# Kernel tuning notes

Measured on AMD Instinct MI355X. Metric: run time of the kernel, lower is better.

## Reference

```python
import jax, jax.numpy as jnp
import numpy as np

EMB = 1024
HEADS = 16


def setup_inputs() -> dict:
    key = jax.random.key(0)
    k1, k2, k3, k4, k5 = jax.random.split(key, 5)
    b, n = 2, 2048
    x = jax.random.normal(k1, (b, n, EMB), dtype=jnp.float32)
    Wqkv = jax.random.normal(k2, (EMB, 3 * EMB), dtype=jnp.float32) * (EMB ** -0.5)
    bqkv = jax.random.normal(k3, (3 * EMB,), dtype=jnp.float32) * 0.02
    Wproj = jax.random.normal(k4, (EMB, EMB), dtype=jnp.float32) * (EMB ** -0.5)
    bproj = jax.random.normal(k5, (EMB,), dtype=jnp.float32) * 0.02
    return {"x": x, "Wqkv": Wqkv, "bqkv": bqkv, "Wproj": Wproj, "bproj": bproj}


def reference(x, Wqkv, bqkv, Wproj, bproj):
    b, n, e = x.shape
    h = HEADS
    d = e // h
    qkv = x @ Wqkv + bqkv                      # [b, n, 3e]
    # rearrange 'b n (h d qkv) -> qkv b h n d' : qkv index is innermost
    qkv = qkv.reshape(b, n, h, d, 3)
    qkv = jnp.transpose(qkv, (4, 0, 2, 1, 3))  # [3, b, h, n, d]
    q, k, v = qkv[0], qkv[1], qkv[2]
    energy = jnp.einsum('bhqd,bhkd->bhqk', q, k)
    scaling = jnp.float32(e) ** 0.5            # NOTE: sqrt(emb_size), not head_dim
    att = jax.nn.softmax(energy / scaling, axis=-1)
    out = jnp.einsum('bhql,bhld->bhqd', att, v)
    out = jnp.transpose(out, (0, 2, 1, 3)).reshape(b, n, e)  # 'b h n d -> b n (h d)'
    return out @ Wproj + bproj
```

## Files before the change

kernel.cpp:

```cpp
#include <hip/hip_runtime.h>
#include <hip/hip_bf16.h>
#include <stdint.h>

typedef __bf16 bf16;
typedef __attribute__((ext_vector_type(8))) __bf16 bf16x8;
typedef __attribute__((ext_vector_type(4))) __bf16 bf16x4;
typedef __attribute__((ext_vector_type(4))) float f32x4;
typedef __attribute__((ext_vector_type(16))) float f32x16;

#define MFMA16(a, b, c) __builtin_amdgcn_mfma_f32_16x16x32_bf16((a), (b), (c), 0, 0, 0)
#define MFMA32(a, b, c) __builtin_amdgcn_mfma_f32_32x32x16_bf16((a), (b), (c), 0, 0, 0)

#define QSCALE 0.045084220027780106f

__device__ __forceinline__ void glds16(const void* g, void* l) {
  __builtin_amdgcn_global_load_lds(
      (const __attribute__((address_space(1))) void*)g,
      (__attribute__((address_space(3))) void*)l, 16, 0, 0);
}

__device__ __forceinline__ bf16x8 ldsfrag(const unsigned char* base, int row, int colb) {
  return *(const bf16x8*)(base + row * 128 + (colb ^ ((row & 7) << 4)));
}

__device__ __forceinline__ uint32_t pkbf16(float a, float b) {
  uint32_t r;
  asm("v_cvt_pk_bf16_f32 %0, %1, %2" : "=v"(r) : "v"(a), "v"(b));
  return r;
}

__device__ __forceinline__ float fexp2(float x) {
#if __has_builtin(__builtin_amdgcn_exp2f)
  return __builtin_amdgcn_exp2f(x);
#else
  float r;
  asm("v_exp_f32 %0, %1" : "=v"(r) : "v"(x));
  return r;
#endif
}

__device__ __forceinline__ f32x16 zero16() {
  f32x16 v;
#pragma unroll
  for (int i = 0; i < 16; ++i) v[i] = 0.f;
  return v;
}

template <int MODE>
__device__ __forceinline__ void prep_w_body(const float* __restrict__ W, bf16* __restrict__ WT,
                                            float (*tile)[256], int c0, int k0) {
  const int C = (MODE == 0) ? 3072 : 1024;
  const int lw = threadIdx.x & 63, w = threadIdx.x >> 6;
#pragma unroll
  for (int i = 0; i < 16; ++i) {
    int r = i * 4 + w;
    f32x4 v = *(const f32x4*)(W + (size_t)(k0 + r) * C + c0 + lw * 4);
    *(f32x4*)&tile[r][lw * 4] = v;
  }
  __syncthreads();
  const int c = c0 + threadIdx.x;
  int j;
  float sc = 1.0f;
  if (MODE == 0) {
    int h = c / 192, rem = c - h * 192, dd = rem / 3, wh = rem - dd * 3;
    j = wh * 1024 + h * 64 + dd;
    if (wh == 0) sc = QSCALE;
  } else {
    j = c;
  }
#pragma unroll
  for (int ch = 0; ch < 8; ++ch) {
    bf16x8 o;
#pragma unroll
    for (int i = 0; i < 8; ++i) o[i] = (bf16)(tile[ch * 8 + i][threadIdx.x] * sc);
    *(bf16x8*)(WT + (size_t)j * 1024 + k0 + ch * 8) = o;
  }
}

__global__ __launch_bounds__(256) void k_prep_all(const float* __restrict__ x,
                                                  const float* __restrict__ Wqkv,
                                                  const float* __restrict__ bqkv,
                                                  const float* __restrict__ Wproj,
                                                  bf16* __restrict__ xb, bf16* __restrict__ WQT,
                                                  bf16* __restrict__ WPT, float* __restrict__ bp) {
  __shared__ float tile[64][256];
  int bid = blockIdx.x;
  if (bid < 2048) {
    int gid = bid * 256 + threadIdx.x;
    const f32x4* xv = (const f32x4*)x;
    f32x4 a = xv[(size_t)gid * 2], b = xv[(size_t)gid * 2 + 1];
    bf16x8 o;
#pragma unroll
    for (int i = 0; i < 4; ++i) { o[i] = (bf16)a[i]; o[i + 4] = (bf16)b[i]; }
    *(bf16x8*)(xb + (size_t)gid * 8) = o;
    return;
  }
  bid -= 2048;
  if (bid < 192) {
    prep_w_body<0>(Wqkv, WQT, tile, (bid % 12) * 256, (bid / 12) * 64);
    return;
  }
  bid -= 192;
  if (bid < 64) {
    prep_w_body<1>(Wproj, WPT, tile, (bid % 4) * 256, (bid / 4) * 64);
    return;
  }
  bid -= 64;
  {
    int gid = bid * 256 + threadIdx.x;
    int wj = gid >> 10, rr = gid & 1023, hh = rr >> 6, d2 = rr & 63;
    float v = bqkv[hh * 192 + d2 * 3 + wj];
    bp[gid] = (wj == 0) ? v * QSCALE : v;
  }
}

__global__ __launch_bounds__(256) void k_gemm_qkv(const bf16* __restrict__ A, const bf16* __restrict__ BT,
                                                  const float* __restrict__ bias, bf16* __restrict__ qk,
                                                  bf16* __restrict__ vt) {
  __shared__ __align__(16) unsigned char sA[16384];
  __shared__ __align__(16) unsigned char sB[16384];
  const int tid = threadIdx.x;
  const int l = tid & 63, w = tid >> 6, g = l >> 4, l15 = l & 15;
  const int wr = w >> 1, wc = w & 1;
  const int wg = (blockIdx.x & 7) * 96 + (blockIdx.x >> 3);
  const int bn = wg % 24, bm = wg / 24;
  const unsigned char* Ab = (const unsigned char*)A + (size_t)bm * 128 * 2048;
  const unsigned char* Bb = (const unsigned char*)BT + (size_t)bn * 128 * 2048;
  f32x4 acc[4][4];
#pragma unroll
  for (int mi = 0; mi < 4; ++mi)
#pragma unroll
    for (int ni = 0; ni < 4; ++ni) acc[mi][ni] = (f32x4){0.f, 0.f, 0.f, 0.f};

  for (int kt = 0; kt < 16; ++kt) {
    const int k0b = kt * 128;
#pragma unroll
    for (int p = 0; p < 4; ++p) {
      int co = (p * 256 + tid) * 16;
      int row = co >> 7, wb = co & 127;
      int sw = wb ^ ((row & 7) << 4);
      glds16(Ab + (size_t)row * 2048 + k0b + sw, sA + co);
      glds16(Bb + (size_t)row * 2048 + k0b + sw, sB + co);
    }
    __syncthreads();
#pragma unroll
    for (int ks = 0; ks < 2; ++ks) {
      bf16x8 af[4], bfr[4];
#pragma unroll
      for (int mi = 0; mi < 4; ++mi) af[mi] = ldsfrag(sA, wr * 64 + mi * 16 + l15, ks * 64 + g * 16);
#pragma unroll
      for (int ni = 0; ni < 4; ++ni) bfr[ni] = ldsfrag(sB, wc * 64 + ni * 16 + l15, ks * 64 + g * 16);
      __builtin_amdgcn_s_setprio(1);
#pragma unroll
      for (int mi = 0; mi < 4; ++mi)
#pragma unroll
        for (int ni = 0; ni < 4; ++ni) acc[mi][ni] = MFMA16(af[mi], bfr[ni], acc[mi][ni]);
      __builtin_amdgcn_s_setprio(0);
    }
    __syncthreads();
  }
#pragma unroll
  for (int ni = 0; ni < 4; ++ni) {
    int j = bn * 128 + wc * 64 + ni * 16 + l15;
    float bj = bias[j];
#pragma unroll
    for (int mi = 0; mi < 4; ++mi) {
      int m0 = bm * 128 + wr * 64 + mi * 16 + g * 4;
      float v[4];
#pragma unroll
      for (int rr = 0; rr < 4; ++rr) v[rr] = acc[mi][ni][rr] + bj;
      int which = j >> 10, r = j & 1023, h = r >> 6, dd = r & 63;
      int b = m0 >> 11, nn = m0 & 2047;
      if (which < 2) {
#pragma unroll
        for (int rr = 0; rr < 4; ++rr)
          qk[(size_t)which * 4194304 + (((size_t)b * 16 + h) * 2048 + nn + rr) * 64 + dd] = (bf16)v[rr];
      } else {
        bf16x4 pw = {(bf16)v[0], (bf16)v[1], (bf16)v[2], (bf16)v[3]};
        *(bf16x4*)(vt + (((size_t)b * 16 + h) * 64 + dd) * 2048 + nn) = pw;
      }
    }
  }
}

__global__ __launch_bounds__(256) void k_gemm_proj(const bf16* __restrict__ A, const bf16* __restrict__ BT,
                                                   const float* __restrict__ bias, float* __restrict__ outf) {
  __shared__ __align__(16) unsigned char sA[8192];
  __shared__ __align__(16) unsigned char sB[16384];
  const int tid = threadIdx.x;
  const int l = tid & 63, w = tid >> 6, g = l >> 4, l15 = l & 15;
  const int wg = (blockIdx.x & 7) * 64 + (blockIdx.x >> 3);
  const int bn = wg & 7, bm = wg >> 3;
  const unsigned char* Ab = (const unsigned char*)A + (size_t)bm * 64 * 2048;
  const unsigned char* Bb = (const unsigned char*)BT + (size_t)bn * 128 * 2048;
  f32x4 acc[4][2];
#pragma unroll
  for (int mi = 0; mi < 4; ++mi)
#pragma unroll
    for (int ni = 0; ni < 2; ++ni) acc[mi][ni] = (f32x4){0.f, 0.f, 0.f, 0.f};

  for (int kt = 0; kt < 16; ++kt) {
    const int k0b = kt * 128;
#pragma unroll
    for (int p = 0; p < 2; ++p) {
      int co = (p * 256 + tid) * 16;
      int row = co >> 7;
      int sw = (co & 127) ^ ((row & 7) << 4);
      glds16(Ab + (size_t)row * 2048 + k0b + sw, sA + co);
    }
#pragma unroll
    for (int p = 0; p < 4; ++p) {
      int co = (p * 256 + tid) * 16;
      int row = co >> 7;
      int sw = (co & 127) ^ ((row & 7) << 4);
      glds16(Bb + (size_t)row * 2048 + k0b + sw, sB + co);
    }
    __syncthreads();
#pragma unroll
    for (int ks = 0; ks < 2; ++ks) {
      bf16x8 af[4], bfr[2];
#pragma unroll
      for (int mi = 0; mi < 4; ++mi) af[mi] = ldsfrag(sA, mi * 16 + l15, ks * 64 + g * 16);
#pragma unroll
      for (int ni = 0; ni < 2; ++ni) bfr[ni] = ldsfrag(sB, w * 32 + ni * 16 + l15, ks * 64 + g * 16);
      __builtin_amdgcn_s_setprio(1);
#pragma unroll
      for (int mi = 0; mi < 4; ++mi)
#pragma unroll
        for (int ni = 0; ni < 2; ++ni) acc[mi][ni] = MFMA16(af[mi], bfr[ni], acc[mi][ni]);
      __builtin_amdgcn_s_setprio(0);
    }
    __syncthreads();
  }
#pragma unroll
  for (int ni = 0; ni < 2; ++ni) {
    int j = bn * 128 + w * 32 + ni * 16 + l15;
    float bj = bias[j];
#pragma unroll
    for (int mi = 0; mi < 4; ++mi) {
      int m0 = bm * 64 + mi * 16 + g * 4;
#pragma unroll
      for (int rr = 0; rr < 4; ++rr) outf[(size_t)(m0 + rr) * 1024 + j] = acc[mi][ni][rr] + bj;
    }
  }
}

__global__ __launch_bounds__(512, 1) void k_attn(const bf16* __restrict__ Qg, const bf16* __restrict__ Kg,
                                                 const bf16* __restrict__ VTg, bf16* __restrict__ Og) {
  __shared__ __align__(16) unsigned char smem[67584];
  const int tid = threadIdx.x;
  const int l = tid & 63, w = tid >> 6;
  const int q = l & 31, hi = l >> 5;
  const int g = w >> 2, wl = w & 3;
  const int stid = tid & 255;

  const int bid = blockIdx.x;
  const int wg = (bid & 7) * 32 + (bid >> 3);
  const int bh = wg >> 3;
  const int q0w = (wg & 7) * 256 + wl * 64;

  bf16x8 qf[2][4];
#pragma unroll
  for (int qt = 0; qt < 2; ++qt)
#pragma unroll
    for (int ks = 0; ks < 4; ++ks)
      qf[qt][ks] = *(const bf16x8*)(Qg + ((size_t)bh * 2048 + q0w + qt * 32 + q) * 64 + ks * 16 + hi * 8);

  f32x16 oacc[2][2];
#pragma unroll
  for (int qt = 0; qt < 2; ++qt) { oacc[qt][0] = zero16(); oacc[qt][1] = zero16(); }
  float lrun4[2][4] = {{0.f, 0.f, 0.f, 0.f}, {0.f, 0.f, 0.f, 0.f}};
  bf16x8 pb[2][4];

  const unsigned char* Kb = (const unsigned char*)Kg + (size_t)bh * 262144 + (size_t)g * 131072;
  const unsigned char* Vb = (const unsigned char*)VTg + (size_t)bh * 262144 + (size_t)g * 2048;
  unsigned char* sKg = smem + g * 16384;
  unsigned char* sVg = smem + 32768 + g * 16384;

  const int co0 = stid * 16, co1 = (256 + stid) * 16;
  const int row0 = co0 >> 7, row1 = co1 >> 7;
  const int sw0 = (co0 & 127) ^ ((row0 & 7) << 4), sw1 = (co1 & 127) ^ ((row1 & 7) << 4);

#define STAGE_K(kb_, buf_)                                                        \
  do {                                                                            \
    const unsigned char* Ksrc = Kb + (size_t)(kb_) * 8192;                        \
    glds16(Ksrc + (co0 & ~127) + sw0, sKg + (buf_) * 8192 + co0);                 \
    glds16(Ksrc + (co1 & ~127) + sw1, sKg + (buf_) * 8192 + co1);                 \
  } while (0)
#define STAGE_V(kb_, buf_)                                                        \
  do {                                                                            \
    glds16(Vb + (size_t)row0 * 4096 + (size_t)(kb_) * 128 + sw0, sVg + (buf_) * 8192 + co0); \
    glds16(Vb + (size_t)row1 * 4096 + (size_t)(kb_) * 128 + sw1, sVg + (buf_) * 8192 + co1); \
  } while (0)

#define QK_EXP_PACK(kbase_)                                                       \
  do {                                                                            \
    _Pragma("unroll") for (int kt = 0; kt < 2; ++kt) {                            \
      bf16x8 kf[4];                                                               \
      _Pragma("unroll") for (int ks = 0; ks < 4; ++ks)                            \
        kf[ks] = ldsfrag((kbase_), kt * 32 + q, ks * 32 + hi * 16);               \
      _Pragma("unroll") for (int qt = 0; qt < 2; ++qt) {                          \
        f32x16 sacc = zero16();                                                   \
        __builtin_amdgcn_s_setprio(1);                                            \
        _Pragma("unroll") for (int ks = 0; ks < 4; ++ks)                          \
          sacc = MFMA32(kf[ks], qf[qt][ks], sacc);                                \
        __builtin_amdgcn_s_setprio(0);                                            \
        float pe[16];                                                             \
        _Pragma("unroll") for (int r = 0; r < 16; ++r) pe[r] = fexp2(sacc[r]);    \
        _Pragma("unroll") for (int m = 0; m < 4; ++m)                             \
          _Pragma("unroll") for (int j = 0; j < 4; ++j) lrun4[qt][j] += pe[4 * m + j]; \
        uint32_t c[4][2];                                                         \
        _Pragma("unroll") for (int m = 0; m < 4; ++m) {                           \
          c[m][0] = pkbf16(pe[4 * m], pe[4 * m + 1]);                             \
          c[m][1] = pkbf16(pe[4 * m + 2], pe[4 * m + 3]);                         \
        }                                                                         \
        _Pragma("unroll") for (int s = 0; s < 2; ++s) {                           \
          uint32_t x0 = c[2 * s][0], y0 = c[2 * s + 1][0];                        \
          uint32_t x1 = c[2 * s][1], y1 = c[2 * s + 1][1];                        \
          asm("v_permlane32_swap_b32 %0, %1" : "+v"(x0), "+v"(y0));               \
          asm("v_permlane32_swap_b32 %0, %1" : "+v"(x1), "+v"(y1));               \
          union { uint32_t u[4]; bf16x8 v; } bfr;                                 \
          bfr.u[0] = x0; bfr.u[1] = x1; bfr.u[2] = y0; bfr.u[3] = y1;             \
          pb[qt][kt * 2 + s] = bfr.v;                                             \
        }                                                                         \
      }                                                                           \
    }                                                                             \
  } while (0)

#define PV_TILE(vbase_)                                                           \
  do {                                                                            \
    __builtin_amdgcn_s_setprio(1);                                                \
    _Pragma("unroll") for (int ks = 0; ks < 4; ++ks)                              \
      _Pragma("unroll") for (int dt = 0; dt < 2; ++dt) {                          \
        bf16x8 vf = ldsfrag((vbase_), dt * 32 + q, ks * 32 + hi * 16);            \
        _Pragma("unroll") for (int qtp = 0; qtp < 2; ++qtp)                       \
          oacc[qtp][dt] = MFMA32(vf, pb[qtp][ks], oacc[qtp][dt]);                 \
      }                                                                           \
    __builtin_amdgcn_s_setprio(0);                                                \
  } while (0)

  STAGE_K(0, 0);
  STAGE_V(0, 0);
  __syncthreads();
  STAGE_K(1, 1);
  QK_EXP_PACK(sKg);
  __syncthreads();
  int cur = 0;

  for (int kb = 0; kb < 15; ++kb) {
    const int nxt = cur ^ 1;
    if (kb < 14) STAGE_K(kb + 2, cur);
    STAGE_V(kb + 1, nxt);
    PV_TILE(sVg + cur * 8192);
    QK_EXP_PACK(sKg + nxt * 8192);
    __syncthreads();
    cur = nxt;
  }
  PV_TILE(sVg + cur * 8192);

#undef STAGE_K
#undef STAGE_V
#undef QK_EXP_PACK
#undef PV_TILE

  float lrun[2];
#pragma unroll
  for (int qt = 0; qt < 2; ++qt)
    lrun[qt] = (lrun4[qt][0] + lrun4[qt][1]) + (lrun4[qt][2] + lrun4[qt][3]);

  float* mbuf = (float*)smem;
  float* lb = (float*)(smem + 65536);
  if (g == 1) {
#pragma unroll
    for (int qt = 0; qt < 2; ++qt) {
#pragma unroll
      for (int dt = 0; dt < 2; ++dt)
#pragma unroll
        for (int r = 0; r < 16; ++r)
          mbuf[((wl * 64 + qt * 32 + dt * 16 + r) << 6) + l] = oacc[qt][dt][r];
      lb[(wl * 2 + qt) * 64 + l] = lrun[qt];
    }
  }
  __syncthreads();
  if (g == 0) {
#pragma unroll
    for (int qt = 0; qt < 2; ++qt)
#pragma unroll
      for (int dt = 0; dt < 2; ++dt)
#pragma unroll
        for (int r = 0; r < 16; ++r)
          oacc[qt][dt][r] += mbuf[((wl * 64 + qt * 32 + dt * 16 + r) << 6) + l];
  }
  __syncthreads();
  if (g == 0) {
    const int b = bh >> 4, h = bh & 15;
    unsigned char* sO = smem + 32768 + wl * 4096;
#pragma unroll
    for (int qt = 0; qt < 2; ++qt) {
      float lr = lrun[qt] + lb[(wl * 2 + qt) * 64 + l];
      float ps = lr + __shfl_xor(lr, 32);
      float linv = 1.0f / ps;
#pragma unroll
      for (int dt = 0; dt < 2; ++dt)
#pragma unroll
        for (int m = 0; m < 4; ++m) {
          uint32_t b0 = pkbf16(oacc[qt][dt][4 * m] * linv, oacc[qt][dt][4 * m + 1] * linv);
          uint32_t b1 = pkbf16(oacc[qt][dt][4 * m + 2] * linv, oacc[qt][dt][4 * m + 3] * linv);
          int byteo = (dt * 64 + m * 16 + hi * 8) ^ ((q & 7) << 4);
          uint32_t* dst = (uint32_t*)(sO + q * 128 + byteo);
          dst[0] = b0; dst[1] = b1;
        }
      const int q0 = q0w + qt * 32;
#pragma unroll
      for (int rd = 0; rd < 4; ++rd) {
        int byteo = hi * 64 + rd * 16;
        bf16x8 v = *(const bf16x8*)(sO + q * 128 + (byteo ^ ((q & 7) << 4)));
        *(bf16x8*)(Og + ((size_t)b * 2048 + q0 + q) * 1024 + h * 64 + byteo / 2) = v;
      }
    }
  }
}

extern "C" void kernel_launch(void* const* d_in, const int* in_sizes, int n_in,
                              void* d_out, int out_size, void* d_ws, size_t ws_size,
                              hipStream_t stream) {
  const float* x = (const float*)d_in[0];
  const float* Wqkv = (const float*)d_in[1];
  const float* bqkv = (const float*)d_in[2];
  const float* Wproj = (const float*)d_in[3];
  const float* bproj = (const float*)d_in[4];
  float* out = (float*)d_out;
  char* ws = (char*)d_ws;

  bf16* XB = (bf16*)(ws + 0);
  bf16* WQT = (bf16*)(ws + 8388608);
  float* BQP = (float*)(ws + 14680064);
  bf16* WPT = (bf16*)(ws + 14696448);
  bf16* Q = (bf16*)(ws + 16793600);
  bf16* K = (bf16*)(ws + 25182208);
  bf16* VT = (bf16*)(ws + 33570816);
  bf16* AO = XB;
  (void)K;
  (void)ws_size;

  k_prep_all<<<2316, 256, 0, stream>>>(x, Wqkv, bqkv, Wproj, XB, WQT, WPT, BQP);
  k_gemm_qkv<<<768, 256, 0, stream>>>(XB, WQT, BQP, Q, VT);
  k_attn<<<256, 512, 0, stream>>>(Q, Q + 4194304, VT, AO);
  k_gemm_proj<<<512, 256, 0, stream>>>(AO, WPT, bproj, out);
}
```

Baseline: 110.3 us.

## Rewrite QKV GEMM as 256x256 tile with 8 waves and double-buffered LDS pipeline

Replaces the 128x128, 4-wave, single-buffered QKV projection GEMM with a 256x256 tile computed by 8 waves using 128KB of LDS. Global-to-LDS loads of the next K-tile are double-buffered and interleaved with four MFMA phases, using explicit vmcnt/lgkmcnt waits and barriers. The aim is to raise data reuse per block and hide load latency behind MFMA work. The cost is one block per CU, only 192 blocks for 256 CUs, and many more barriers.

```diff
diff --git a/kernel.cpp b/kernel.cpp
--- a/kernel.cpp
+++ b/kernel.cpp
@@ -114,62 +114,148 @@
   }
 }
 
-__global__ __launch_bounds__(256) void k_gemm_qkv(const bf16* __restrict__ A, const bf16* __restrict__ BT,
-                                                  const float* __restrict__ bias, bf16* __restrict__ qk,
-                                                  bf16* __restrict__ vt) {
-  __shared__ __align__(16) unsigned char sA[16384];
-  __shared__ __align__(16) unsigned char sB[16384];
+__global__ __launch_bounds__(512, 1) void k_gemm_qkv8(const bf16* __restrict__ A,
+                                                      const bf16* __restrict__ BT,
+                                                      const float* __restrict__ bias,
+                                                      bf16* __restrict__ qk, bf16* __restrict__ vt) {
+  __shared__ __align__(16) unsigned char smem[131072];
+  unsigned char* sA = smem;
+  unsigned char* sB = smem + 65536;
   const int tid = threadIdx.x;
   const int l = tid & 63, w = tid >> 6, g = l >> 4, l15 = l & 15;
-  const int wr = w >> 1, wc = w & 1;
-  const int wg = (blockIdx.x & 7) * 96 + (blockIdx.x >> 3);
-  const int bn = wg % 24, bm = wg / 24;
-  const unsigned char* Ab = (const unsigned char*)A + (size_t)bm * 128 * 2048;
-  const unsigned char* Bb = (const unsigned char*)BT + (size_t)bn * 128 * 2048;
-  f32x4 acc[4][4];
-#pragma unroll
-  for (int mi = 0; mi < 4; ++mi)
+  const int wr = w >> 2, wc = w & 3;
+  const int wg = (blockIdx.x & 7) * 24 + (blockIdx.x >> 3);
+  const int bn = wg % 12, bm = wg / 12;
+  const unsigned char* Ab = (const unsigned char*)A + (size_t)bm * 256 * 2048;
+  const unsigned char* Bb = (const unsigned char*)BT + (size_t)bn * 256 * 2048;
+
+  f32x4 acc[8][4];
+#pragma unroll
+  for (int mi = 0; mi < 8; ++mi)
 #pragma unroll
     for (int ni = 0; ni < 4; ++ni) acc[mi][ni] = (f32x4){0.f, 0.f, 0.f, 0.f};
 
-  for (int kt = 0; kt < 16; ++kt) {
-    const int k0b = kt * 128;
-#pragma unroll
-    for (int p = 0; p < 4; ++p) {
-      int co = (p * 256 + tid) * 16;
-      int row = co >> 7, wb = co & 127;
-      int sw = wb ^ ((row & 7) << 4);
-      glds16(Ab + (size_t)row * 2048 + k0b + sw, sA + co);
-      glds16(Bb + (size_t)row * 2048 + k0b + sw, sB + co);
-    }
-    __syncthreads();
-#pragma unroll
-    for (int ks = 0; ks < 2; ++ks) {
-      bf16x8 af[4], bfr[4];
-#pragma unroll
-      for (int mi = 0; mi < 4; ++mi) af[mi] = ldsfrag(sA, wr * 64 + mi * 16 + l15, ks * 64 + g * 16);
-#pragma unroll
-      for (int ni = 0; ni < 4; ++ni) bfr[ni] = ldsfrag(sB, wc * 64 + ni * 16 + l15, ks * 64 + g * 16);
-      __builtin_amdgcn_s_setprio(1);
-#pragma unroll
-      for (int mi = 0; mi < 4; ++mi)
-#pragma unroll
-        for (int ni = 0; ni < 4; ++ni) acc[mi][ni] = MFMA16(af[mi], bfr[ni], acc[mi][ni]);
-      __builtin_amdgcn_s_setprio(0);
-    }
-    __syncthreads();
-  }
+  const int co0 = tid * 16, co1 = tid * 16 + 8192;
+  const int r0 = co0 >> 7, r1 = co1 >> 7;
+  const int s0 = (co0 & 127) ^ ((r0 & 7) << 4), s1 = (co1 & 127) ^ ((r1 & 7) << 4);
+
+#define STG(gbase_, KT_, H_, ldsb_, BUF_)                                                   \
+  do {                                                                                      \
+    glds16((gbase_) + (size_t)((H_)*128 + r0) * 2048 + (size_t)(KT_)*128 + s0,              \
+           (ldsb_) + (BUF_)*32768 + (H_)*16384 + co0);                                      \
+    glds16((gbase_) + (size_t)((H_)*128 + r1) * 2048 + (size_t)(KT_)*128 + s1,              \
+           (ldsb_) + (BUF_)*32768 + (H_)*16384 + co1);                                      \
+  } while (0)
+
+#define VMWAIT(n)                                                                           \
+  do {                                                                                      \
+    asm volatile("s_waitcnt vmcnt(" #n ")" ::: "memory");                                   \
+    __builtin_amdgcn_sched_barrier(0);                                                      \
+  } while (0)
+#define RAWBAR()                                                                            \
+  do {                                                                                      \
+    __builtin_amdgcn_sched_barrier(0);                                                      \
+    __builtin_amdgcn_s_barrier();                                                           \
+    __builtin_amdgcn_sched_barrier(0);                                                      \
+  } while (0)
+#define LGKM0()                                                                             \
+  do {                                                                                      \
+    asm volatile("s_waitcnt lgkmcnt(0)" ::: "memory");                                      \
+    __builtin_amdgcn_sched_barrier(0);                                                      \
+  } while (0)
+
+#define PH_MFMA(P_)                                                                         \
+  do {                                                                                      \
+    __builtin_amdgcn_s_setprio(1);                                                          \
+    _Pragma("unroll") for (int ks = 0; ks < 2; ++ks)                                        \
+      _Pragma("unroll") for (int m2 = 0; m2 < 2; ++m2)                                      \
+        _Pragma("unroll") for (int ni = 0; ni < 4; ++ni)                                    \
+          acc[(P_)*2 + m2][ni] = MFMA16(af[m2][ks], bfr[ni][ks], acc[(P_)*2 + m2][ni]);     \
+    __builtin_amdgcn_s_setprio(0);                                                          \
+  } while (0)
+
+#define RD_AF(P_, BUF_)                                                                     \
+  do {                                                                                      \
+    _Pragma("unroll") for (int m2 = 0; m2 < 2; ++m2)                                        \
+      _Pragma("unroll") for (int ks = 0; ks < 2; ++ks)                                      \
+        af[m2][ks] = ldsfrag(sA + (BUF_)*32768, wr * 128 + ((P_)*2 + m2) * 16 + l15,        \
+                             ks * 64 + g * 16);                                             \
+  } while (0)
+
+#define ITER(T_, PBUF_, DOA_, DOB_, FULLVM_)                                                \
+  do {                                                                                      \
+    bf16x8 bfr[4][2];                                                                       \
+    bf16x8 af[2][2];                                                                        \
+                                \
+    _Pragma("unroll") for (int ni = 0; ni < 4; ++ni)                                        \
+      _Pragma("unroll") for (int ks = 0; ks < 2; ++ks)                                      \
+        bfr[ni][ks] = ldsfrag(sB + (PBUF_)*32768, wc * 64 + ni * 16 + l15, ks * 64 + g * 16); \
+    RD_AF(0, PBUF_);                                                                        \
+    if (DOA_) STG(Ab, (T_) + 1, 0, sA, 1 - (PBUF_));                                        \
+    RAWBAR();                                                                               \
+    LGKM0();                                                                                \
+    PH_MFMA(0);                                                                             \
+    RAWBAR();                                                                               \
+                                        \
+    RD_AF(1, PBUF_);                                                                        \
+    if (DOA_) STG(Ab, (T_) + 1, 1, sA, 1 - (PBUF_));                                        \
+    if (DOB_) STG(Bb, (T_) + 2, 0, sB, (PBUF_));                                            \
+    RAWBAR();                                                                               \
+    LGKM0();                                                                                \
+    PH_MFMA(1);                                                                             \
+    RAWBAR();                                                                               \
+                                                   \
+    RD_AF(2, PBUF_);                                                                        \
+    if (DOB_) STG(Bb, (T_) + 2, 1, sB, (PBUF_));                                            \
+    RAWBAR();                                                                               \
+    LGKM0();                                                                                \
+    PH_MFMA(2);                                                                             \
+    RAWBAR();                                                                               \
+                            \
+    RD_AF(3, PBUF_);                                                                        \
+    if (FULLVM_) { VMWAIT(4); } else { VMWAIT(0); }                                         \
+    RAWBAR();                                                                               \
+    LGKM0();                                                                                \
+    PH_MFMA(3);                                                                             \
+    RAWBAR();                                                                               \
+  } while (0)
+
+  STG(Ab, 0, 0, sA, 0);
+  STG(Ab, 0, 1, sA, 0);
+  STG(Bb, 0, 0, sB, 0);
+  STG(Bb, 0, 1, sB, 0);
+  STG(Bb, 1, 0, sB, 1);
+  STG(Bb, 1, 1, sB, 1);
+  VMWAIT(4);
+  RAWBAR();
+
+  for (int t2 = 0; t2 < 7; ++t2) {
+    const int t = t2 * 2;
+    ITER(t, 0, 1, 1, 1);
+    ITER(t + 1, 1, 1, 1, 1);
+  }
+  ITER(14, 0, 1, 0, 0);
+  ITER(15, 1, 0, 0, 0);
+
+#undef STG
+#undef VMWAIT
+#undef RAWBAR
+#undef LGKM0
+#undef PH_MFMA
+#undef RD_AF
+#undef ITER
+
 #pragma unroll
   for (int ni = 0; ni < 4; ++ni) {
-    int j = bn * 128 + wc * 64 + ni * 16 + l15;
+    int j = bn * 256 + wc * 64 + ni * 16 + l15;
     float bj = bias[j];
-#pragma unroll
-    for (int mi = 0; mi < 4; ++mi) {
-      int m0 = bm * 128 + wr * 64 + mi * 16 + g * 4;
+    int which = j >> 10, r = j & 1023, h = r >> 6, dd = r & 63;
+#pragma unroll
+    for (int mi = 0; mi < 8; ++mi) {
+      int m0 = bm * 256 + wr * 128 + mi * 16 + g * 4;
       float v[4];
 #pragma unroll
       for (int rr = 0; rr < 4; ++rr) v[rr] = acc[mi][ni][rr] + bj;
-      int which = j >> 10, r = j & 1023, h = r >> 6, dd = r & 63;
       int b = m0 >> 11, nn = m0 & 2047;
       if (which < 2) {
 #pragma unroll
@@ -444,7 +530,7 @@
   (void)ws_size;
 
   k_prep_all<<<2316, 256, 0, stream>>>(x, Wqkv, bqkv, Wproj, XB, WQT, WPT, BQP);
-  k_gemm_qkv<<<768, 256, 0, stream>>>(XB, WQT, BQP, Q, VT);
+  k_gemm_qkv8<<<192, 512, 0, stream>>>(XB, WQT, BQP, Q, VT);
   k_attn<<<256, 512, 0, stream>>>(Q, Q + 4194304, VT, AO);
   k_gemm_proj<<<512, 256, 0, stream>>>(AO, WPT, bproj, out);
 }
```

After: 109.8 us. About the same (-0.5%).
